# Kernel optimization log

Measured on AMD Instinct MI355X. Metric: run time of the kernel, lower is better.

The kernel has to match this reference:

```python
import jax, jax.numpy as jnp
import numpy as np

N, T, c = 8192, 121, 40
C, P = 384, 12

def setup_inputs() -> dict:
    key = jax.random.key(0)
    k1, k2, k3 = jax.random.split(key, 3)
    waveforms = jax.random.normal(k1, (N, T, c), dtype=jnp.float32)
    max_channels = jax.random.randint(k2, (N,), 0, C, dtype=jnp.int64)
    # values in [0, c]; value == c indexes the inf pad column (no parent)
    parents_index = jax.random.randint(k3, (C, c, P), 0, c + 1, dtype=jnp.int64)
    return {"waveforms": waveforms, "max_channels": max_channels, "parents_index": parents_index}

def reference(waveforms, max_channels, parents_index):
    n = waveforms.shape[0]
    # peak-to-peak per channel: [N, c]
    ptps = waveforms.max(axis=1) - waveforms.min(axis=1)
    # pad with +inf sentinel column so missing parents never bind the min
    pad_ptps = jnp.pad(ptps, ((0, 0), (0, 1)), constant_values=jnp.inf)  # [N, c+1]
    pidx = parents_index[max_channels]                                   # [N, c, P]
    parent_ptps = pad_ptps[jnp.arange(n)[:, None, None], pidx]           # [N, c, P]
    parent_min_ptps = parent_ptps.min(axis=2)                            # [N, c]
    rescaling = jnp.minimum(parent_min_ptps / ptps, 1.0)                 # [N, c]
    decreasing_ptps = ptps * rescaling
    decreasing_waveforms = waveforms * rescaling[:, None, :]
    return decreasing_waveforms, decreasing_ptps
```

## Files before the change

### kernel.cpp

```cpp
#include <hip/hip_runtime.h>
#include <math.h>


#define N_T 121
#define N_C 40
#define N_P 12
#define TPB 256
#define WF_ELEMS (N_T * N_C)
#define WF_QUADS (WF_ELEMS / 4)
#define FULL_K   (WF_QUADS / TPB)
#define TAIL_Q   (WF_QUADS - FULL_K * TPB)
#define NBLK 1024
#define SPB  8

typedef float f32x4 __attribute__((ext_vector_type(4)));

#define GLOAD_LDS16(g, l)                                              \
    __builtin_amdgcn_global_load_lds(                                  \
        (const __attribute__((address_space(1))) void*)(g),            \
        (__attribute__((address_space(3))) void*)(l), 16, 0, 0)

#define BAR_LGKM() do {                                                \
    asm volatile("s_waitcnt lgkmcnt(0)" ::: "memory");                 \
    __builtin_amdgcn_s_barrier();                                      \
} while (0)

__device__ __forceinline__ void stage(const float* __restrict__ src,
                                      float* dst, int tid) {
    #pragma unroll
    for (int k = 0; k < FULL_K; ++k) {
        const int q = tid + TPB * k;
        GLOAD_LDS16(src + 4 * q, dst + 4 * q);
    }
    if (tid < TAIL_Q) {
        const int q = FULL_K * TPB + tid;
        GLOAD_LDS16(src + 4 * q, dst + 4 * q);
    }
}

__global__ __launch_bounds__(TPB, 4) void enforce_decrease_kernel(
    const float* __restrict__ waveforms,
    const int*   __restrict__ max_channels,
    const int*   __restrict__ parents_index,
    float*       __restrict__ out,
    int n_total)
{
    __shared__ float wf[2][WF_ELEMS];
    __shared__ float pmx[4 * N_C];
    __shared__ float pmn[4 * N_C];
    __shared__ float ptp[N_C];
    __shared__ float resc[N_C];

    const int tid = threadIdx.x;
    const int bid = blockIdx.x;

    stage(waveforms + (size_t)bid * WF_ELEMS, wf[0], tid);

    for (int g = 0; g < SPB; ++g) {
        const int    n    = bid + g * NBLK;
        float*       wcur = wf[g & 1];

        __syncthreads();

        if (g + 1 < SPB)
            stage(waveforms + (size_t)(n + NBLK) * WF_ELEMS, wf[(g + 1) & 1], tid);

        if (tid < 4 * N_C) {
            const int ch = tid % N_C;
            const int g4 = tid / N_C;
            float mx = -INFINITY, mn = INFINITY;
            for (int t = g4; t < N_T; t += 4) {
                const float v = wcur[t * N_C + ch];
                mx = fmaxf(mx, v);
                mn = fminf(mn, v);
            }
            pmx[tid] = mx;
            pmn[tid] = mn;
        }
        BAR_LGKM();

        if (tid < N_C) {
            float mx = pmx[tid], mn = pmn[tid];
            #pragma unroll
            for (int q = 1; q < 4; ++q) {
                mx = fmaxf(mx, pmx[q * N_C + tid]);
                mn = fminf(mn, pmn[q * N_C + tid]);
            }
            ptp[tid] = mx - mn;
        }
        BAR_LGKM();

        if (tid < N_C) {
            const int  mc   = max_channels[n];
            const int* prow = parents_index + mc * (N_C * N_P) + tid * N_P;
            float minp = INFINITY;
            #pragma unroll
            for (int p = 0; p < N_P; ++p) {
                const int idx = prow[p];
                minp = fminf(minp, (idx >= N_C) ? INFINITY : ptp[idx]);
            }
            const float r = fminf(minp / ptp[tid], 1.0f);
            resc[tid] = r;
            __builtin_nontemporal_store(
                ptp[tid] * r,
                out + (size_t)n_total * WF_ELEMS + (size_t)n * N_C + tid);
        }
        BAR_LGKM();

        const f32x4* w4   = (const f32x4*)wcur;
        f32x4*       dst4 = (f32x4*)(out + (size_t)n * WF_ELEMS);
        #pragma unroll
        for (int k = 0; k < FULL_K; ++k) {
            const int i = tid + TPB * k;
            f32x4 v = w4[i];
            const int ch0 = (i * 4) % N_C;
            v.x *= resc[ch0];
            v.y *= resc[ch0 + 1];
            v.z *= resc[ch0 + 2];
            v.w *= resc[ch0 + 3];
            __builtin_nontemporal_store(v, &dst4[i]);
        }
        if (tid < TAIL_Q) {
            const int i = FULL_K * TPB + tid;
            f32x4 v = w4[i];
            const int ch0 = (i * 4) % N_C;
            v.x *= resc[ch0];
            v.y *= resc[ch0 + 1];
            v.z *= resc[ch0 + 2];
            v.w *= resc[ch0 + 3];
            __builtin_nontemporal_store(v, &dst4[i]);
        }
    }
}

extern "C" void kernel_launch(void* const* d_in, const int* in_sizes, int n_in,
                              void* d_out, int out_size, void* d_ws, size_t ws_size,
                              hipStream_t stream) {
    const float* waveforms     = (const float*)d_in[0];
    const int*   max_channels  = (const int*)d_in[1];
    const int*   parents_index = (const int*)d_in[2];
    float*       out           = (float*)d_out;

    const int n = in_sizes[1];

    enforce_decrease_kernel<<<dim3(NBLK), dim3(TPB), 0, stream>>>(
        waveforms, max_channels, parents_index, out, n);
}
```

Before: 58.24 us.

## Double block size and use partial vmcnt waits for async LDS staging

Result: faster. 56.13 us (-3.6%).

```diff
diff --git a/kernel.cpp b/kernel.cpp
--- a/kernel.cpp
+++ b/kernel.cpp
@@ -5,13 +5,13 @@
 #define N_T 121
 #define N_C 40
 #define N_P 12
-#define TPB 256
+#define TPB 512
+#define NBLK 1024
+#define SPB 8
 #define WF_ELEMS (N_T * N_C)
 #define WF_QUADS (WF_ELEMS / 4)
-#define FULL_K   (WF_QUADS / TPB)
-#define TAIL_Q   (WF_QUADS - FULL_K * TPB)
-#define NBLK 1024
-#define SPB  8
+#define TAIL_Q   (WF_QUADS - 2 * TPB)
+#define ROW_F    4864
 
 typedef float f32x4 __attribute__((ext_vector_type(4)));
 
@@ -27,25 +27,20 @@
 
 __device__ __forceinline__ void stage(const float* __restrict__ src,
                                       float* dst, int tid) {
-    #pragma unroll
-    for (int k = 0; k < FULL_K; ++k) {
-        const int q = tid + TPB * k;
-        GLOAD_LDS16(src + 4 * q, dst + 4 * q);
-    }
-    if (tid < TAIL_Q) {
-        const int q = FULL_K * TPB + tid;
-        GLOAD_LDS16(src + 4 * q, dst + 4 * q);
-    }
+    GLOAD_LDS16(src + 4 * tid,         dst + 4 * tid);
+    GLOAD_LDS16(src + 4 * (TPB + tid), dst + 4 * (TPB + tid));
+    const int q2 = (tid < TAIL_Q) ? (2 * TPB + tid) : (tid - TAIL_Q);
+    GLOAD_LDS16(src + 4 * q2, dst + 4 * q2);
 }
 
-__global__ __launch_bounds__(TPB, 4) void enforce_decrease_kernel(
+__global__ __launch_bounds__(TPB, 8) void enforce_decrease_kernel(
     const float* __restrict__ waveforms,
     const int*   __restrict__ max_channels,
     const int*   __restrict__ parents_index,
     float*       __restrict__ out,
     int n_total)
 {
-    __shared__ float wf[2][WF_ELEMS];
+    __shared__ float wf[2][ROW_F];
     __shared__ float pmx[4 * N_C];
     __shared__ float pmn[4 * N_C];
     __shared__ float ptp[N_C];
@@ -57,13 +52,18 @@
     stage(waveforms + (size_t)bid * WF_ELEMS, wf[0], tid);
 
     for (int g = 0; g < SPB; ++g) {
-        const int    n    = bid + g * NBLK;
-        float*       wcur = wf[g & 1];
+        const int n    = bid + g * NBLK;
+        float*    wcur = wf[g & 1];
 
-        __syncthreads();
+        if (g == 0)
+            asm volatile("s_waitcnt vmcnt(0) lgkmcnt(0)" ::: "memory");
+        else
+            asm volatile("s_waitcnt vmcnt(2) lgkmcnt(0)" ::: "memory");
+        __builtin_amdgcn_s_barrier();
 
         if (g + 1 < SPB)
-            stage(waveforms + (size_t)(n + NBLK) * WF_ELEMS, wf[(g + 1) & 1], tid);
+            stage(waveforms + (size_t)(n + NBLK) * WF_ELEMS,
+                  wf[(g + 1) & 1], tid);
 
         if (tid < 4 * N_C) {
             const int ch = tid % N_C;
@@ -109,9 +109,8 @@
 
         const f32x4* w4   = (const f32x4*)wcur;
         f32x4*       dst4 = (f32x4*)(out + (size_t)n * WF_ELEMS);
-        #pragma unroll
-        for (int k = 0; k < FULL_K; ++k) {
-            const int i = tid + TPB * k;
+        if (tid < TAIL_Q) {
+            const int i = 2 * TPB + tid;
             f32x4 v = w4[i];
             const int ch0 = (i * 4) % N_C;
             v.x *= resc[ch0];
@@ -120,8 +119,9 @@
             v.w *= resc[ch0 + 3];
             __builtin_nontemporal_store(v, &dst4[i]);
         }
-        if (tid < TAIL_Q) {
-            const int i = FULL_K * TPB + tid;
+        #pragma unroll
+        for (int k = 0; k < 2; ++k) {
+            const int i = tid + TPB * k;
             f32x4 v = w4[i];
             const int ch0 = (i * 4) % N_C;
             v.x *= resc[ch0];
```
